# Optimization experiments

Measured on AMD Instinct MI355X. Metric: run time of the kernel, lower is better.

The kernel has to match this reference:

```python
import jax, jax.numpy as jnp
import numpy as np

# Static configuration (matches init_kwargs)
EMBED_DIM = 256
NUM_HEADS = 8
NUM_LEVELS = 4
NUM_POINTS = 16
N_DEGREE = 3
HEAD_DIM = EMBED_DIM // NUM_HEADS
SPATIAL_SHAPES = ((64, 64), (32, 32), (16, 16), (8, 8))  # (H, W) per level
LEN_V = sum(h * w for h, w in SPATIAL_SHAPES)


def _bilinear_gather(v, loc, Hl, Wl):
    """Bilinear sampling with zero padding, align_corners=False.
    v:   [bs, nH, Hl*Wl, hd]  flattened level feature map (per head)
    loc: [bs, nH, Q, 2]       (x, y) in [0, 1]
    returns [bs, nH, Q, hd]
    """
    x = loc[..., 0] * Wl - 0.5
    y = loc[..., 1] * Hl - 0.5
    x0 = jnp.floor(x)
    y0 = jnp.floor(y)
    wx = x - x0
    wy = y - y0
    out = jnp.zeros(v.shape[:2] + (loc.shape[2], v.shape[-1]), v.dtype)
    corners = ((0, 0, (1 - wx) * (1 - wy)), (1, 0, wx * (1 - wy)),
               (0, 1, (1 - wx) * wy), (1, 1, wx * wy))
    for dx, dy, w in corners:
        xi = x0 + dx
        yi = y0 + dy
        valid = (xi >= 0) & (xi < Wl) & (yi >= 0) & (yi < Hl)
        idx = (jnp.clip(yi, 0, Hl - 1) * Wl + jnp.clip(xi, 0, Wl - 1)).astype(jnp.int32)
        g = jnp.take_along_axis(v, idx[..., None], axis=2)  # [bs,nH,Q,hd]
        out = out + g * (w * valid.astype(w.dtype))[..., None]
    return out


def setup_inputs() -> dict:
    key = jax.random.key(0)
    ks = jax.random.split(key, 12)
    bs, Lq = 4, 1024
    s = 0.02
    return {
        "query": jax.random.normal(ks[0], (bs, Lq, EMBED_DIM), jnp.float32),
        # polynomial coefficients for x(l), y(l); scaled so curves stay roughly in [0,1]
        "reference_points": jax.random.uniform(ks[1], (bs, Lq, 2 * (N_DEGREE + 1)), jnp.float32) * 0.25,
        "value": jax.random.normal(ks[2], (bs, LEN_V, EMBED_DIM), jnp.float32),
        "W_value": jax.random.normal(ks[3], (EMBED_DIM, EMBED_DIM), jnp.float32) * s,
        "b_value": jnp.zeros((EMBED_DIM,), jnp.float32),
        "W_offsets": jax.random.normal(ks[4], (EMBED_DIM, NUM_HEADS * NUM_LEVELS * NUM_POINTS * 2), jnp.float32) * s,
        "b_offsets": jax.random.normal(ks[5], (NUM_HEADS * NUM_LEVELS * NUM_POINTS * 2,), jnp.float32) * 0.5,
        "W_attn": jax.random.normal(ks[6], (EMBED_DIM, NUM_HEADS * NUM_LEVELS * NUM_POINTS), jnp.float32) * s,
        "b_attn": jnp.zeros((NUM_HEADS * NUM_LEVELS * NUM_POINTS,), jnp.float32),
        "W_out": jax.random.normal(ks[7], (EMBED_DIM, EMBED_DIM), jnp.float32) * s,
        "b_out": jnp.zeros((EMBED_DIM,), jnp.float32),
    }


def reference(query, reference_points, value, W_value, b_value, W_offsets,
              b_offsets, W_attn, b_attn, W_out, b_out):
    bs, Lq, _ = query.shape
    Lv = value.shape[1]
    nH, nL, nP, hd = NUM_HEADS, NUM_LEVELS, NUM_POINTS, HEAD_DIM

    v = (value @ W_value + b_value).reshape(bs, Lv, nH, hd)

    sampling_offsets = (query @ W_offsets + b_offsets).reshape(bs, Lq, nH, nL, nP, 2)
    attn = jax.nn.softmax((query @ W_attn + b_attn).reshape(bs, Lq, nH, nL * nP), axis=-1)
    attn = attn.reshape(bs, Lq, nH, nL, nP)

    # reference_points last dim == 8: polynomial branch
    lambdaz = jnp.linspace(0.0, 1.0, nP)
    lambdas = jnp.stack([lambdaz ** i for i in range(N_DEGREE, -1, -1)], axis=1)  # [nP, deg+1]
    ref_polys = reference_points.reshape(bs, Lq, 2, N_DEGREE + 1)
    pnts = jnp.einsum('bqcd,pd->bqpc', ref_polys, lambdas)  # [bs,Lq,nP,2] (x,y)

    # offset_normalizer: spatial shapes flipped -> (W, H) per level
    normalizer = jnp.array([[w, h] for (h, w) in SPATIAL_SHAPES], jnp.float32)
    normalizer = normalizer.reshape(1, 1, 1, nL, 1, 2)
    sampling_locations = pnts[:, :, None, None, :, :] + sampling_offsets / normalizer
    # -> [bs, Lq, nH, nL, nP, 2] in [0,1]

    # deformable attention core: per-level bilinear gather + softmax-weighted sum
    out = jnp.zeros((bs, Lq, nH, hd), v.dtype)
    start = 0
    for lvl, (Hl, Wl) in enumerate(SPATIAL_SHAPES):
        v_l = v[:, start:start + Hl * Wl].transpose(0, 2, 1, 3)  # [bs,nH,Hl*Wl,hd]
        loc_l = sampling_locations[:, :, :, lvl]                 # [bs,Lq,nH,nP,2]
        loc_l = loc_l.transpose(0, 2, 1, 3, 4).reshape(bs, nH, Lq * nP, 2)
        sampled = _bilinear_gather(v_l, loc_l, Hl, Wl).reshape(bs, nH, Lq, nP, hd)
        out = out + jnp.einsum('bhqpd,bqhp->bqhd', sampled, attn[:, :, :, lvl])
        start += Hl * Wl

    output = out.reshape(bs, Lq, nH * hd) @ W_out + b_out
    return output, sampling_locations, attn
```

## Files before the change

kernel.cpp:

```cpp
#include <hip/hip_runtime.h>
#include <math.h>

#define BS 4
#define LQ 1024
#define EMB 256
#define NH 8
#define NL 4
#define NP 16
#define HD 32
#define LV 5440
#define KDIM 256

typedef __attribute__((ext_vector_type(8))) short short8;
typedef __attribute__((ext_vector_type(4))) float f32x4;

__device__ inline unsigned short f2bf(float f) {
    unsigned u = __builtin_bit_cast(unsigned, f);
    u += 0x7fff + ((u >> 16) & 1);
    return (unsigned short)(u >> 16);
}

__global__ __launch_bounds__(256) void convT_all(const float* __restrict__ Wv,
                                                 const float* __restrict__ Wo,
                                                 const float* __restrict__ Wa,
                                                 const float* __restrict__ Wu,
                                                 unsigned short* __restrict__ Wt) {
    __shared__ float tile[32][33];
    const int n0 = blockIdx.x * 32, k0 = blockIdx.y * 32;
    const float* src; int N, nloc;
    if (n0 < 256)       { src = Wv; N = 256;  nloc = n0; }
    else if (n0 < 1280) { src = Wo; N = 1024; nloc = n0 - 256; }
    else if (n0 < 1792) { src = Wa; N = 512;  nloc = n0 - 1280; }
    else                { src = Wu; N = 256;  nloc = n0 - 1792; }
    const int tx = threadIdx.x & 31, ty = threadIdx.x >> 5;
#pragma unroll
    for (int i = 0; i < 32; i += 8)
        tile[ty + i][tx] = src[(size_t)(k0 + ty + i) * N + nloc + tx];
    __syncthreads();
#pragma unroll
    for (int i = 0; i < 32; i += 8)
        Wt[(size_t)(n0 + ty + i) * KDIM + k0 + tx] = f2bf(tile[tx][ty + i]);
}

template <bool A_FP32, int MODE>
__global__ __launch_bounds__(256) void gemm128(const void* __restrict__ Aptr,
                                               const unsigned short* __restrict__ Bt,
                                               const float* __restrict__ bias,
                                               const float* __restrict__ bias2,
                                               const float* __restrict__ refp,
                                               float* __restrict__ C,
                                               float* __restrict__ C2,
                                               int N) {
    __shared__ short As[128 * 32];
    __shared__ short Bs[128 * 32];
    const int t = threadIdx.x;
    const int lane = t & 63, w = t >> 6;
    const int quad = lane >> 4, l16 = lane & 15;
    const int wr = w >> 1, wc = w & 1;
    const int row0 = blockIdx.y * 128, col0 = blockIdx.x * 128;

    f32x4 acc[4][4] = {};

    const int bro = t >> 2, bko = (t & 3) * 8;
    const unsigned short* bsrc0 = Bt + (size_t)(col0 + bro) * KDIM + bko;
    const unsigned short* bsrc1 = bsrc0 + (size_t)64 * KDIM;
    short* const bdst0 = Bs + (size_t)(w * 64) * 8;
    short* const bdst1 = Bs + (size_t)(256 + w * 64) * 8;

    const int ar = t >> 1, akq = (t & 1) * 16;
    const float* afsrc = (const float*)Aptr + (size_t)(row0 + ar) * KDIM + akq;
    short* const adst = As + ar * 32 + akq;
    const unsigned short* absrc0 = (const unsigned short*)Aptr + (size_t)(row0 + bro) * KDIM + bko;
    const unsigned short* absrc1 = absrc0 + (size_t)64 * KDIM;
    short* const adst0 = As + (size_t)(w * 64) * 8;
    short* const adst1 = As + (size_t)(256 + w * 64) * 8;

    for (int kt = 0; kt < KDIM / 32; ++kt) {
        __syncthreads();
        __builtin_amdgcn_global_load_lds(
            (const __attribute__((address_space(1))) void*)(bsrc0 + kt * 32),
            (__attribute__((address_space(3))) void*)bdst0, 16, 0, 0);
        __builtin_amdgcn_global_load_lds(
            (const __attribute__((address_space(1))) void*)(bsrc1 + kt * 32),
            (__attribute__((address_space(3))) void*)bdst1, 16, 0, 0);
        if (A_FP32) {
            const float* s = afsrc + kt * 32;
            const float4 f0 = *(const float4*)(s);
            const float4 f1 = *(const float4*)(s + 4);
            const float4 f2 = *(const float4*)(s + 8);
            const float4 f3 = *(const float4*)(s + 12);
            short8 h0, h1;
            h0[0] = (short)f2bf(f0.x); h0[1] = (short)f2bf(f0.y);
            h0[2] = (short)f2bf(f0.z); h0[3] = (short)f2bf(f0.w);
            h0[4] = (short)f2bf(f1.x); h0[5] = (short)f2bf(f1.y);
            h0[6] = (short)f2bf(f1.z); h0[7] = (short)f2bf(f1.w);
            h1[0] = (short)f2bf(f2.x); h1[1] = (short)f2bf(f2.y);
            h1[2] = (short)f2bf(f2.z); h1[3] = (short)f2bf(f2.w);
            h1[4] = (short)f2bf(f3.x); h1[5] = (short)f2bf(f3.y);
            h1[6] = (short)f2bf(f3.z); h1[7] = (short)f2bf(f3.w);
            *(short8*)(adst)     = h0;
            *(short8*)(adst + 8) = h1;
        } else {
            __builtin_amdgcn_global_load_lds(
                (const __attribute__((address_space(1))) void*)(absrc0 + kt * 32),
                (__attribute__((address_space(3))) void*)adst0, 16, 0, 0);
            __builtin_amdgcn_global_load_lds(
                (const __attribute__((address_space(1))) void*)(absrc1 + kt * 32),
                (__attribute__((address_space(3))) void*)adst1, 16, 0, 0);
        }
        __syncthreads();

        short8 af[4], bf[4];
#pragma unroll
        for (int mi = 0; mi < 4; ++mi)
            af[mi] = *(const short8*)&As[(wr * 64 + mi * 16 + l16) * 32 + quad * 8];
#pragma unroll
        for (int ni = 0; ni < 4; ++ni)
            bf[ni] = *(const short8*)&Bs[(wc * 64 + ni * 16 + l16) * 32 + quad * 8];
#pragma unroll
        for (int mi = 0; mi < 4; ++mi)
#pragma unroll
            for (int ni = 0; ni < 4; ++ni)
                acc[mi][ni] = __builtin_amdgcn_mfma_f32_16x16x32_bf16(af[mi], bf[ni],
                                                                      acc[mi][ni], 0, 0, 0);
    }

    if (MODE == 0) {
#pragma unroll
        for (int ni = 0; ni < 4; ++ni) {
            const int c = col0 + wc * 64 + ni * 16 + l16;
            const float bv = bias[c];
#pragma unroll
            for (int mi = 0; mi < 4; ++mi) {
                const int r0 = row0 + wr * 64 + mi * 16 + quad * 4;
#pragma unroll
                for (int rr = 0; rr < 4; ++rr)
                    C[(size_t)(r0 + rr) * N + c] = acc[mi][ni][rr] + bv;
            }
        }
    } else {
        const bool is_off = (col0 < 1024);
#pragma unroll
        for (int ni = 0; ni < 4; ++ni) {
            const int cg = col0 + wc * 64 + ni * 16 + l16;
            if (is_off) {
                const int xy = cg & 1, p = (cg >> 1) & 15, l = (cg >> 5) & 3;
                const float lam = (float)p * (1.0f / 15.0f);
                const float l2 = lam * lam, l3 = l2 * lam;
                const float rW = (l == 0) ? 0.015625f : (l == 1) ? 0.03125f
                                : (l == 2) ? 0.0625f : 0.125f;
                const float bv = bias[cg];
#pragma unroll
                for (int mi = 0; mi < 4; ++mi) {
                    const int r0 = row0 + wr * 64 + mi * 16 + quad * 4;
#pragma unroll
                    for (int rr = 0; rr < 4; ++rr) {
                        const int r = r0 + rr;
                        const float4 rp = *(const float4*)(refp + (size_t)r * 8 + xy * 4);
                        const float poly = rp.x * l3 + rp.y * l2 + rp.z * lam + rp.w;
                        C[(size_t)r * 1024 + cg] = poly + (acc[mi][ni][rr] + bv) * rW;
                    }
                }
            } else {
                const int ca = cg - 1024;
                const float bv = bias2[ca];
#pragma unroll
                for (int mi = 0; mi < 4; ++mi) {
                    const int r0 = row0 + wr * 64 + mi * 16 + quad * 4;
#pragma unroll
                    for (int rr = 0; rr < 4; ++rr)
                        C2[(size_t)(r0 + rr) * 512 + ca] = acc[mi][ni][rr] + bv;
                }
            }
        }
    }
}

__global__ __launch_bounds__(256) void softmax64(float* __restrict__ a) {
    const int row  = blockIdx.x * 4 + (threadIdx.x >> 6);
    const int lane = threadIdx.x & 63;
    float* p = a + (size_t)row * 64 + lane;
    float v = *p;
    float m = v;
#pragma unroll
    for (int off = 32; off; off >>= 1) m = fmaxf(m, __shfl_xor(m, off));
    float e = expf(v - m);
    float s = e;
#pragma unroll
    for (int off = 32; off; off >>= 1) s += __shfl_xor(s, off);
    *p = e / s;
}

__global__ __launch_bounds__(256) void sample_kernel(const float* __restrict__ v,
                                                     const float* __restrict__ loc,
                                                     const float* __restrict__ attn,
                                                     unsigned short* __restrict__ interm) {
    const int t = threadIdx.x;
    const int g = blockIdx.x * 8 + (t >> 5);
    const int lane32 = t & 31;
    const int l8 = lane32 & 7;
    const int lvl = lane32 >> 3;
    const int h = g & 7, bq = g >> 3, b = bq >> 10;

    const int W = 64 >> lvl;
    const float Wf = (float)W;
    const int sh = 6 - lvl;
    const int start = (lvl == 0) ? 0 : (lvl == 1) ? 4096 : (lvl == 2) ? 5120 : 5376;

    const float* lp = loc  + (size_t)g * 128 + lvl * 32;
    const float* ap = attn + (size_t)g * 64  + lvl * 16;
    const float* vl = v + (size_t)b * LV * EMB + (size_t)start * EMB + h * HD + l8 * 4;

    float ax = 0.f, ay = 0.f, az = 0.f, aw = 0.f;

    auto point = [&](float lx, float ly, float wt) {
        const float x = lx * Wf - 0.5f, y = ly * Wf - 0.5f;
        const float x0f = floorf(x), y0f = floorf(y);
        const float wx = x - x0f, wy = y - y0f;
        const int x0 = (int)x0f, y0 = (int)y0f;
        const int x1 = x0 + 1, y1 = y0 + 1;
        const float iwx = 1.f - wx, iwy = 1.f - wy;
        float w00 = iwx * iwy * wt, w10 = wx * iwy * wt;
        float w01 = iwx * wy * wt,  w11 = wx * wy * wt;
        const bool vx0 = (x0 >= 0) & (x0 < W);
        const bool vx1 = (x1 >= 0) & (x1 < W);
        const bool vy0 = (y0 >= 0) & (y0 < W);
        const bool vy1 = (y1 >= 0) & (y1 < W);
        w00 = (vx0 & vy0) ? w00 : 0.f;
        w10 = (vx1 & vy0) ? w10 : 0.f;
        w01 = (vx0 & vy1) ? w01 : 0.f;
        w11 = (vx1 & vy1) ? w11 : 0.f;
        const int cx0 = min(max(x0, 0), W - 1);
        const int cx1 = min(max(x1, 0), W - 1);
        const int cy0 = min(max(y0, 0), W - 1);
        const int cy1 = min(max(y1, 0), W - 1);
        const float4 g00 = *(const float4*)(vl + (size_t)((cy0 << sh) + cx0) * EMB);
        const float4 g10 = *(const float4*)(vl + (size_t)((cy0 << sh) + cx1) * EMB);
        const float4 g01 = *(const float4*)(vl + (size_t)((cy1 << sh) + cx0) * EMB);
        const float4 g11 = *(const float4*)(vl + (size_t)((cy1 << sh) + cx1) * EMB);
        ax += w00 * g00.x + w10 * g10.x + w01 * g01.x + w11 * g11.x;
        ay += w00 * g00.y + w10 * g10.y + w01 * g01.y + w11 * g11.y;
        az += w00 * g00.z + w10 * g10.z + w01 * g01.z + w11 * g11.z;
        aw += w00 * g00.w + w10 * g10.w + w01 * g01.w + w11 * g11.w;
    };

#pragma unroll
    for (int p4 = 0; p4 < 16; p4 += 4) {
        const float4 la = *(const float4*)(lp + 2 * p4);
        const float4 lb = *(const float4*)(lp + 2 * p4 + 4);
        const float4 wv = *(const float4*)(ap + p4);
        point(la.x, la.y, wv.x); point(la.z, la.w, wv.y);
        point(lb.x, lb.y, wv.z); point(lb.z, lb.w, wv.w);
    }

#pragma unroll
    for (int m = 8; m <= 16; m <<= 1) {
        ax += __shfl_xor(ax, m); ay += __shfl_xor(ay, m);
        az += __shfl_xor(az, m); aw += __shfl_xor(aw, m);
    }

    if (lvl == 0) {
        unsigned short o[4] = {f2bf(ax), f2bf(ay), f2bf(az), f2bf(aw)};
        *(ushort4*)(interm + (size_t)bq * EMB + h * HD + l8 * 4) = *(const ushort4*)o;
    }
}

extern "C" void kernel_launch(void* const* d_in, const int* in_sizes, int n_in,
                              void* d_out, int out_size, void* d_ws, size_t ws_size,
                              hipStream_t stream) {
    const float* query   = (const float*)d_in[0];
    const float* refp    = (const float*)d_in[1];
    const float* value   = (const float*)d_in[2];
    const float* W_value = (const float*)d_in[3];
    const float* b_value = (const float*)d_in[4];
    const float* W_off   = (const float*)d_in[5];
    const float* b_off   = (const float*)d_in[6];
    const float* W_attn  = (const float*)d_in[7];
    const float* b_attn  = (const float*)d_in[8];
    const float* W_out   = (const float*)d_in[9];
    const float* b_out   = (const float*)d_in[10];

    float* out      = (float*)d_out;
    float* loc_out  = out + 1048576;
    float* attn_out = out + 5242880;

    char* ws = (char*)d_ws;
    float*          v_proj = (float*)ws;
    unsigned short* interm = (unsigned short*)(ws + 22282240);
    unsigned short* Wt_all = (unsigned short*)(ws + 24379392);

    const dim3 blk(256);

    convT_all<<<dim3(2048 / 32, 8), blk, 0, stream>>>(W_value, W_off, W_attn, W_out, Wt_all);

    gemm128<true, 0><<<dim3(2, 170), blk, 0, stream>>>(
        value, Wt_all, b_value, nullptr, nullptr, v_proj, nullptr, 256);

    gemm128<true, 1><<<dim3(12, 32), blk, 0, stream>>>(
        query, Wt_all + (size_t)256 * KDIM, b_off, b_attn, refp, loc_out, attn_out, 1536);

    softmax64<<<(BS * LQ * NH) / 4, blk, 0, stream>>>(attn_out);

    sample_kernel<<<(BS * LQ * NH) / 8, blk, 0, stream>>>(v_proj, loc_out, attn_out, interm);

    gemm128<false, 0><<<dim3(2, 32), blk, 0, stream>>>(
        interm, Wt_all + (size_t)1792 * KDIM, b_out, nullptr, nullptr, out, nullptr, 256);
}
```

Measured before the change: 184.7 us.

## Fuse softmax into attention GEMM epilogue and store projected values as bf16

The attention-logit GEMM epilogue now computes the per-row softmax over 64 columns with cross-lane shuffles, so the separate softmax kernel and its extra global round trip are gone. The value projection writes bf16 instead of fp32, which halves the bytes the sampling kernel gathers. The sampler now uses 16 lanes per (query, head), each loading 8 bf16 channels per corner. This lowers precision of the sampled values and relies on each 64-wide softmax row lying inside a single wave's 4x16 tile.

```diff
diff --git a/kernel.cpp b/kernel.cpp
--- a/kernel.cpp
+++ b/kernel.cpp
@@ -48,7 +48,7 @@
                                                const float* __restrict__ bias,
                                                const float* __restrict__ bias2,
                                                const float* __restrict__ refp,
-                                               float* __restrict__ C,
+                                               void* __restrict__ Cv,
                                                float* __restrict__ C2,
                                                int N) {
     __shared__ short As[128 * 32];
@@ -125,7 +125,7 @@
                                                                       acc[mi][ni], 0, 0, 0);
     }
 
-    if (MODE == 0) {
+    if (MODE == 0 || MODE == 2) {
 #pragma unroll
         for (int ni = 0; ni < 4; ++ni) {
             const int c = col0 + wc * 64 + ni * 16 + l16;
@@ -134,16 +134,20 @@
             for (int mi = 0; mi < 4; ++mi) {
                 const int r0 = row0 + wr * 64 + mi * 16 + quad * 4;
 #pragma unroll
-                for (int rr = 0; rr < 4; ++rr)
-                    C[(size_t)(r0 + rr) * N + c] = acc[mi][ni][rr] + bv;
+                for (int rr = 0; rr < 4; ++rr) {
+                    const float o = acc[mi][ni][rr] + bv;
+                    if (MODE == 0) ((float*)Cv)[(size_t)(r0 + rr) * N + c] = o;
+                    else ((unsigned short*)Cv)[(size_t)(r0 + rr) * N + c] = f2bf(o);
+                }
             }
         }
     } else {
         const bool is_off = (col0 < 1024);
-#pragma unroll
-        for (int ni = 0; ni < 4; ++ni) {
-            const int cg = col0 + wc * 64 + ni * 16 + l16;
-            if (is_off) {
+        if (is_off) {
+            float* C = (float*)Cv;
+#pragma unroll
+            for (int ni = 0; ni < 4; ++ni) {
+                const int cg = col0 + wc * 64 + ni * 16 + l16;
                 const int xy = cg & 1, p = (cg >> 1) & 15, l = (cg >> 5) & 3;
                 const float lam = (float)p * (1.0f / 15.0f);
                 const float l2 = lam * lam, l3 = l2 * lam;
@@ -161,45 +165,50 @@
                         C[(size_t)r * 1024 + cg] = poly + (acc[mi][ni][rr] + bv) * rW;
                     }
                 }
-            } else {
-                const int ca = cg - 1024;
-                const float bv = bias2[ca];
-#pragma unroll
-                for (int mi = 0; mi < 4; ++mi) {
-                    const int r0 = row0 + wr * 64 + mi * 16 + quad * 4;
-#pragma unroll
-                    for (int rr = 0; rr < 4; ++rr)
-                        C2[(size_t)(r0 + rr) * 512 + ca] = acc[mi][ni][rr] + bv;
+            }
+        } else {
+            const int cabase = col0 - 1024 + wc * 64;
+            float bv[4];
+#pragma unroll
+            for (int ni = 0; ni < 4; ++ni) bv[ni] = bias2[cabase + ni * 16 + l16];
+#pragma unroll
+            for (int mi = 0; mi < 4; ++mi) {
+                const int r0 = row0 + wr * 64 + mi * 16 + quad * 4;
+#pragma unroll
+                for (int rr = 0; rr < 4; ++rr) {
+                    float v0 = acc[mi][0][rr] + bv[0];
+                    float v1 = acc[mi][1][rr] + bv[1];
+                    float v2 = acc[mi][2][rr] + bv[2];
+                    float v3 = acc[mi][3][rr] + bv[3];
+                    float mx = fmaxf(fmaxf(v0, v1), fmaxf(v2, v3));
+#pragma unroll
+                    for (int mk = 1; mk < 16; mk <<= 1) mx = fmaxf(mx, __shfl_xor(mx, mk));
+                    v0 = __expf(v0 - mx); v1 = __expf(v1 - mx);
+                    v2 = __expf(v2 - mx); v3 = __expf(v3 - mx);
+                    float s = v0 + v1 + v2 + v3;
+#pragma unroll
+                    for (int mk = 1; mk < 16; mk <<= 1) s += __shfl_xor(s, mk);
+                    const float inv = 1.0f / s;
+                    const size_t rb = (size_t)(r0 + rr) * 512 + cabase + l16;
+                    C2[rb]      = v0 * inv;
+                    C2[rb + 16] = v1 * inv;
+                    C2[rb + 32] = v2 * inv;
+                    C2[rb + 48] = v3 * inv;
                 }
             }
         }
     }
 }
 
-__global__ __launch_bounds__(256) void softmax64(float* __restrict__ a) {
-    const int row  = blockIdx.x * 4 + (threadIdx.x >> 6);
-    const int lane = threadIdx.x & 63;
-    float* p = a + (size_t)row * 64 + lane;
-    float v = *p;
-    float m = v;
-#pragma unroll
-    for (int off = 32; off; off >>= 1) m = fmaxf(m, __shfl_xor(m, off));
-    float e = expf(v - m);
-    float s = e;
-#pragma unroll
-    for (int off = 32; off; off >>= 1) s += __shfl_xor(s, off);
-    *p = e / s;
-}
-
-__global__ __launch_bounds__(256) void sample_kernel(const float* __restrict__ v,
+__global__ __launch_bounds__(256) void sample_kernel(const unsigned short* __restrict__ v,
                                                      const float* __restrict__ loc,
                                                      const float* __restrict__ attn,
                                                      unsigned short* __restrict__ interm) {
     const int t = threadIdx.x;
-    const int g = blockIdx.x * 8 + (t >> 5);
-    const int lane32 = t & 31;
-    const int l8 = lane32 & 7;
-    const int lvl = lane32 >> 3;
+    const int g = blockIdx.x * 16 + (t >> 4);
+    const int l16 = t & 15;
+    const int lvl = l16 >> 2;
+    const int cq  = l16 & 3;
     const int h = g & 7, bq = g >> 3, b = bq >> 10;
 
     const int W = 64 >> lvl;
@@ -209,9 +218,20 @@
 
     const float* lp = loc  + (size_t)g * 128 + lvl * 32;
     const float* ap = attn + (size_t)g * 64  + lvl * 16;
-    const float* vl = v + (size_t)b * LV * EMB + (size_t)start * EMB + h * HD + l8 * 4;
-
-    float ax = 0.f, ay = 0.f, az = 0.f, aw = 0.f;
+    const unsigned short* vl = v + ((size_t)b * LV + start) * EMB + h * HD + cq * 8;
+
+    float acc[8] = {};
+
+    auto cadd = [&](uint4 q, float wgt) {
+        const unsigned dw[4] = {q.x, q.y, q.z, q.w};
+#pragma unroll
+        for (int k = 0; k < 4; ++k) {
+            const float lo = __builtin_bit_cast(float, dw[k] << 16);
+            const float hi = __builtin_bit_cast(float, dw[k] & 0xffff0000u);
+            acc[2 * k]     = fmaf(wgt, lo, acc[2 * k]);
+            acc[2 * k + 1] = fmaf(wgt, hi, acc[2 * k + 1]);
+        }
+    };
 
     auto point = [&](float lx, float ly, float wt) {
         const float x = lx * Wf - 0.5f, y = ly * Wf - 0.5f;
@@ -222,10 +242,10 @@
         const float iwx = 1.f - wx, iwy = 1.f - wy;
         float w00 = iwx * iwy * wt, w10 = wx * iwy * wt;
         float w01 = iwx * wy * wt,  w11 = wx * wy * wt;
-        const bool vx0 = (x0 >= 0) & (x0 < W);
-        const bool vx1 = (x1 >= 0) & (x1 < W);
-        const bool vy0 = (y0 >= 0) & (y0 < W);
-        const bool vy1 = (y1 >= 0) & (y1 < W);
+        const bool vx0 = (unsigned)x0 < (unsigned)W;
+        const bool vx1 = (unsigned)x1 < (unsigned)W;
+        const bool vy0 = (unsigned)y0 < (unsigned)W;
+        const bool vy1 = (unsigned)y1 < (unsigned)W;
         w00 = (vx0 & vy0) ? w00 : 0.f;
         w10 = (vx1 & vy0) ? w10 : 0.f;
         w01 = (vx0 & vy1) ? w01 : 0.f;
@@ -234,14 +254,11 @@
         const int cx1 = min(max(x1, 0), W - 1);
         const int cy0 = min(max(y0, 0), W - 1);
         const int cy1 = min(max(y1, 0), W - 1);
-        const float4 g00 = *(const float4*)(vl + (size_t)((cy0 << sh) + cx0) * EMB);
-        const float4 g10 = *(const float4*)(vl + (size_t)((cy0 << sh) + cx1) * EMB);
-        const float4 g01 = *(const float4*)(vl + (size_t)((cy1 << sh) + cx0) * EMB);
-        const float4 g11 = *(const float4*)(vl + (size_t)((cy1 << sh) + cx1) * EMB);
-        ax += w00 * g00.x + w10 * g10.x + w01 * g01.x + w11 * g11.x;
-        ay += w00 * g00.y + w10 * g10.y + w01 * g01.y + w11 * g11.y;
-        az += w00 * g00.z + w10 * g10.z + w01 * g01.z + w11 * g11.z;
-        aw += w00 * g00.w + w10 * g10.w + w01 * g01.w + w11 * g11.w;
+        const uint4 g00 = *(const uint4*)(vl + (size_t)((cy0 << sh) + cx0) * EMB);
+        const uint4 g10 = *(const uint4*)(vl + (size_t)((cy0 << sh) + cx1) * EMB);
+        const uint4 g01 = *(const uint4*)(vl + (size_t)((cy1 << sh) + cx0) * EMB);
+        const uint4 g11 = *(const uint4*)(vl + (size_t)((cy1 << sh) + cx1) * EMB);
+        cadd(g00, w00); cadd(g10, w10); cadd(g01, w01); cadd(g11, w11);
     };
 
 #pragma unroll
@@ -254,14 +271,15 @@
     }
 
 #pragma unroll
-    for (int m = 8; m <= 16; m <<= 1) {
-        ax += __shfl_xor(ax, m); ay += __shfl_xor(ay, m);
-        az += __shfl_xor(az, m); aw += __shfl_xor(aw, m);
-    }
+    for (int m = 4; m <= 8; m <<= 1)
+#pragma unroll
+        for (int k = 0; k < 8; ++k) acc[k] += __shfl_xor(acc[k], m);
 
     if (lvl == 0) {
-        unsigned short o[4] = {f2bf(ax), f2bf(ay), f2bf(az), f2bf(aw)};
-        *(ushort4*)(interm + (size_t)bq * EMB + h * HD + l8 * 4) = *(const ushort4*)o;
+        unsigned short o[8];
+#pragma unroll
+        for (int k = 0; k < 8; ++k) o[k] = f2bf(acc[k]);
+        *(uint4*)(interm + (size_t)bq * EMB + h * HD + cq * 8) = *(const uint4*)o;
     }
 }
 
@@ -285,23 +303,21 @@
     float* attn_out = out + 5242880;
 
     char* ws = (char*)d_ws;
-    float*          v_proj = (float*)ws;
-    unsigned short* interm = (unsigned short*)(ws + 22282240);
-    unsigned short* Wt_all = (unsigned short*)(ws + 24379392);
+    unsigned short* v_proj = (unsigned short*)ws;
+    unsigned short* interm = (unsigned short*)(ws + 11141120);
+    unsigned short* Wt_all = (unsigned short*)(ws + 13238272);
 
     const dim3 blk(256);
 
     convT_all<<<dim3(2048 / 32, 8), blk, 0, stream>>>(W_value, W_off, W_attn, W_out, Wt_all);
 
-    gemm128<true, 0><<<dim3(2, 170), blk, 0, stream>>>(
+    gemm128<true, 2><<<dim3(2, 170), blk, 0, stream>>>(
         value, Wt_all, b_value, nullptr, nullptr, v_proj, nullptr, 256);
 
     gemm128<true, 1><<<dim3(12, 32), blk, 0, stream>>>(
         query, Wt_all + (size_t)256 * KDIM, b_off, b_attn, refp, loc_out, attn_out, 1536);
 
-    softmax64<<<(BS * LQ * NH) / 4, blk, 0, stream>>>(attn_out);
-
-    sample_kernel<<<(BS * LQ * NH) / 8, blk, 0, stream>>>(v_proj, loc_out, attn_out, interm);
+    sample_kernel<<<(BS * LQ * NH) / 16, blk, 0, stream>>>(v_proj, loc_out, attn_out, interm);
 
     gemm128<false, 0><<<dim3(2, 32), blk, 0, stream>>>(
         interm, Wt_all + (size_t)1792 * KDIM, b_out, nullptr, nullptr, out, nullptr, 256);
```

Measured after the change: 352.6 us. 90.9% more time.
